# Optimization experiments

Measured on AMD Instinct MI355X. Metric: run time of the kernel, lower is better.

The kernel has to match this reference:

```python
import jax, jax.numpy as jnp
import numpy as np

EPS = 1e-5  # float32 path of the torch LayerNorm variants


def setup_inputs() -> dict:
    key = jax.random.key(0)
    ks = jax.random.split(key, 12)
    b, c, t, h, w = 2, 512, 16, 32, 32
    heads, dim_head = 8, 64
    inner = heads * dim_head            # 512
    cpb = c // 2                        # 256 (ContinuousPositionBias hidden dim)
    inner_ff = int(c * 4 * 2 / 3)       # 1365 (GEGLU FeedForward)
    s = 0.02
    return {
        "x": jax.random.normal(ks[0], (b, c, t, h, w), jnp.float32),
        "framerate": 4,
        "g_norm": jnp.ones((c,), jnp.float32),
        "Wq": jax.random.normal(ks[1], (c, inner), jnp.float32) * s,
        "Wkv": jax.random.normal(ks[2], (c, 2 * inner), jnp.float32) * s,
        "Wo": jax.random.normal(ks[3], (inner, c), jnp.float32) * s,
        "pos_emb": jax.random.normal(ks[4], (1, 30, c), jnp.float32),
        "fr_emb": jax.random.normal(ks[5], (1, 30, c), jnp.float32),
        "cpb_w1": jax.random.normal(ks[6], (1, cpb), jnp.float32) * s,
        "cpb_b1": jnp.zeros((cpb,), jnp.float32),
        "cpb_w2": jax.random.normal(ks[7], (cpb, cpb), jnp.float32) * s,
        "cpb_b2": jnp.zeros((cpb,), jnp.float32),
        "cpb_w3": jax.random.normal(ks[8], (cpb, 8), jnp.float32) * s,
        "cpb_b3": jnp.zeros((8,), jnp.float32),
        "Win": jax.random.normal(ks[9], (c, 2 * inner_ff), jnp.float32) * s,
        "chan_g": jnp.ones((inner_ff,), jnp.float32),
        "Wout": jax.random.normal(ks[10], (inner_ff, c), jnp.float32) * s,
    }


def _forward(x, framerate, g_norm, Wq, Wkv, Wo, pos_emb, fr_emb,
             cpb_w1, cpb_b1, cpb_w2, cpb_b2, cpb_w3, cpb_b3,
             Win, chan_g, Wout):
    b, c, t, hh, ww = x.shape
    heads = cpb_b3.shape[0]
    dim_head = Wq.shape[1] // heads
    scale = dim_head ** -0.5

    # ---- ContinuousPositionBias over time (num_dims=1, log_dist) ----
    pos = jnp.arange(t)
    rel = (pos[:, None] - pos[None, :])[..., None].astype(x.dtype)   # [t, t, 1]
    rel = jnp.sign(rel) * jnp.log(jnp.abs(rel) + 1.0)
    hb = jax.nn.silu(rel @ cpb_w1 + cpb_b1)
    hb = jax.nn.silu(hb @ cpb_w2 + cpb_b2)
    bias = jnp.transpose(hb @ cpb_w3 + cpb_b3, (2, 0, 1))            # [H, t, t]

    # ---- temporal attention: fold spatial dims into batch ----
    xt = jnp.transpose(x, (0, 3, 4, 2, 1)).reshape(b * hh * ww, t, c)  # [B, t, c]
    xe = xt + pos_emb[:, :t] + fr_emb[:, framerate - 1:framerate]
    # LayerNorm as written in the source: stats over dim=1 (the token axis)
    mean = jnp.mean(xe, axis=1, keepdims=True)
    var = jnp.var(xe, axis=1, keepdims=True)
    xn = (xe - mean) * jax.lax.rsqrt(jnp.maximum(var, EPS)) * g_norm

    q = (xn @ Wq).reshape(-1, t, heads, dim_head).transpose(0, 2, 1, 3)  # [B,H,t,d]
    k, v = jnp.split(xn @ Wkv, 2, axis=-1)
    k = k.reshape(-1, t, heads, dim_head).transpose(0, 2, 1, 3)
    v = v.reshape(-1, t, heads, dim_head).transpose(0, 2, 1, 3)

    sim = jnp.einsum('bhid,bhjd->bhij', q * scale, k) + bias[None]
    attn = jax.nn.softmax(sim, axis=-1)
    o = jnp.einsum('bhij,bhjd->bhid', attn, v)
    o = o.transpose(0, 2, 1, 3).reshape(-1, t, heads * dim_head) @ Wo
    xt = o + xt  # residual
    x = jnp.transpose(xt.reshape(b, hh, ww, t, c), (0, 4, 3, 1, 2))  # [b,c,t,h,w]

    # ---- GEGLU FeedForward (1x1x1 convs) with token shift over time ----
    y = jnp.einsum('bcthw,co->bothw', x, Win)
    y1, gate = jnp.split(y, 2, axis=1)
    y = y1 * jax.nn.gelu(gate, approximate=False)
    half = (y.shape[1] + 1) // 2  # torch.chunk: first chunk gets ceil
    ya, yb = y[:, :half], y[:, half:]
    yb = jnp.pad(yb, ((0, 0), (0, 0), (1, 0), (0, 0), (0, 0)))[:, :, :-1]
    y = jnp.concatenate([ya, yb], axis=1)
    m = jnp.mean(y, axis=1, keepdims=True)
    vv = jnp.var(y, axis=1, keepdims=True)
    y = (y - m) * jax.lax.rsqrt(jnp.maximum(vv, EPS)) * chan_g[None, :, None, None, None]
    y = jnp.einsum('bcthw,co->bothw', y, Wout)
    return y + x


def reference(x, framerate, g_norm, Wq, Wkv, Wo, pos_emb, fr_emb,
              cpb_w1, cpb_b1, cpb_w2, cpb_b2, cpb_w3, cpb_b3,
              Win, chan_g, Wout):
    return _forward(x, framerate, g_norm, Wq, Wkv, Wo, pos_emb, fr_emb,
                    cpb_w1, cpb_b1, cpb_w2, cpb_b2, cpb_w3, cpb_b3,
                    Win, chan_g, Wout)
```

## Files before the change

### kernel.cpp

```cpp
#include <hip/hip_runtime.h>

using u16 = unsigned short;
using f32x4 = __attribute__((ext_vector_type(4))) float;
using short8 = __attribute__((ext_vector_type(8))) short;

__device__ __forceinline__ float bf2f(u16 u) {
    union { unsigned int i; float f; } v; v.i = ((unsigned int)u) << 16; return v.f;
}
__device__ __forceinline__ u16 f2bf(float f) {
    union { float f; unsigned int i; } v; v.f = f;
    unsigned int u = v.i;
    u += 0x7fffu + ((u >> 16) & 1u);
    return (u16)(u >> 16);
}
__device__ __forceinline__ void gload16(const u16* g, u16* l) {
    __builtin_amdgcn_global_load_lds((const __attribute__((address_space(1))) void*)g,
                                     (__attribute__((address_space(3))) void*)l, 16, 0, 0);
}

__global__ __launch_bounds__(256) void prep_weights(
    const float* __restrict__ Wq, const float* __restrict__ Wkv,
    const float* __restrict__ Wo, const float* __restrict__ Win,
    const float* __restrict__ Wout, const float* __restrict__ cg,
    u16* __restrict__ wqkvt, u16* __restrict__ wot,
    u16* __restrict__ winp, u16* __restrict__ woutt)
{
    int i = blockIdx.x * 256 + threadIdx.x;
    if (i < 1536 * 512) {
        int n = i >> 9, c = i & 511;
        float v = (n < 512) ? Wq[c * 512 + n] : Wkv[c * 1024 + (n - 512)];
        wqkvt[i] = f2bf(v); return;
    }
    i -= 1536 * 512;
    if (i < 512 * 512) {
        int cc = i >> 9, k = i & 511;
        wot[i] = f2bf(Wo[k * 512 + cc]); return;
    }
    i -= 512 * 512;
    if (i < 2816 * 512) {
        int n = i >> 9, c = i & 511;
        int jj = ((n >> 5) << 4) + (n & 15);
        int gate = (n >> 4) & 1;
        float v = (jj < 1365) ? Win[c * 2730 + jj + gate * 1365] : 0.f;
        winp[i] = f2bf(v); return;
    }
    i -= 2816 * 512;
    if (i < 512 * 1408) {
        int cc = i / 1408, j = i % 1408;
        float v = (j < 1365) ? Wout[j * 512 + cc] * cg[j] : 0.f;
        woutt[i] = f2bf(v); return;
    }
}

__global__ __launch_bounds__(64) void ssum_kernel(
    const float* __restrict__ Wout, const float* __restrict__ cg, float* __restrict__ ssum)
{
    int c = blockIdx.x;
    int lane = threadIdx.x;
    float s = 0.f;
    for (int j = lane; j < 1365; j += 64) s += Wout[j * 512 + c] * cg[j];
    for (int off = 32; off; off >>= 1) s += __shfl_xor(s, off);
    if (lane == 0) ssum[c] = s;
}

__global__ __launch_bounds__(256) void bias_kernel(
    const float* __restrict__ w1, const float* __restrict__ b1,
    const float* __restrict__ w2, const float* __restrict__ b2,
    const float* __restrict__ w3, const float* __restrict__ b3,
    float* __restrict__ bias)
{
    __shared__ float h1[256], h2[256];
    int rc = blockIdx.x;
    int ti = rc >> 4, tj = rc & 15;
    int j = threadIdx.x;
    float r = (float)(ti - tj);
    float rl = (r > 0.f) ? logf(r + 1.f) : ((r < 0.f) ? -logf(1.f - r) : 0.f);
    float a = rl * w1[j] + b1[j];
    h1[j] = a / (1.f + __expf(-a));
    __syncthreads();
    float acc = b2[j];
    for (int k = 0; k < 256; ++k) acc += h1[k] * w2[k * 256 + j];
    h2[j] = acc / (1.f + __expf(-acc));
    __syncthreads();
    if (j < 8) {
        float ab = b3[j];
        for (int k = 0; k < 256; ++k) ab += h2[k] * w3[k * 8 + j];
        bias[j * 256 + ti * 16 + tj] = ab;
    }
}

__global__ __launch_bounds__(256) void k1_norm(
    const float* __restrict__ x, const int* __restrict__ frp,
    const float* __restrict__ g_norm, const float* __restrict__ pos_emb,
    const float* __restrict__ fr_emb,
    u16* __restrict__ xn, u16* __restrict__ xt)
{
    __shared__ u16 tile[256 * 34];
    const int bid = blockIdx.x;
    const int b = bid >> 10, rem = bid & 1023;
    const int hw0 = (rem >> 4) << 4;
    const int c0 = (rem & 15) << 5;
    const int tid = threadIdx.x;
    const int hwl = tid & 15, cl = tid >> 4;
    const int fr = frp[0] - 1;
    float v[2][16], mean2[2], ri2[2], gg2[2], fv2[2];
    for (int cp = 0; cp < 2; ++cp) {
        const int c = c0 + cl + (cp << 4);
        const float* xp = x + (size_t)(b * 512 + c) * 16384 + hw0 + hwl;
        const float fv = fr_emb[fr * 512 + c];
        float s1 = 0.f, s2 = 0.f;
#pragma unroll
        for (int t = 0; t < 16; ++t) {
            float xv = xp[t * 1024];
            v[cp][t] = xv;
            float xe = xv + pos_emb[t * 512 + c] + fv;
            s1 += xe; s2 += xe * xe;
        }
        float m = s1 * 0.0625f;
        float var = s2 * 0.0625f - m * m;
        mean2[cp] = m; ri2[cp] = rsqrtf(fmaxf(var, 1e-5f));
        gg2[cp] = g_norm[c]; fv2[cp] = fv;
    }
    for (int cp = 0; cp < 2; ++cp) {
        const int c = c0 + cl + (cp << 4);
#pragma unroll
        for (int t = 0; t < 16; ++t) {
            float xe = v[cp][t] + pos_emb[t * 512 + c] + fv2[cp];
            tile[((t << 4) + hwl) * 34 + cl + (cp << 4)] = f2bf((xe - mean2[cp]) * ri2[cp] * gg2[cp]);
        }
    }
    __syncthreads();
    for (int it = 0; it < 32; ++it) {
        int rowl = (tid >> 5) + (it << 3);
        int col = tid & 31;
        size_t p = (size_t)b * 16384 + (size_t)(rowl >> 4) * 1024 + hw0 + (rowl & 15);
        xn[p * 512 + c0 + col] = tile[rowl * 34 + col];
    }
    __syncthreads();
    for (int cp = 0; cp < 2; ++cp)
#pragma unroll
        for (int t = 0; t < 16; ++t)
            tile[((t << 4) + hwl) * 34 + cl + (cp << 4)] = f2bf(v[cp][t]);
    __syncthreads();
    for (int it = 0; it < 32; ++it) {
        int rowl = (tid >> 5) + (it << 3);
        int col = tid & 31;
        size_t p = (size_t)b * 16384 + (size_t)(rowl >> 4) * 1024 + hw0 + (rowl & 15);
        xt[p * 512 + c0 + col] = tile[rowl * 34 + col];
    }
}

template<int EPI>
__global__ __launch_bounds__(256, 2) void gemm_bt(
    const u16* __restrict__ A, const u16* __restrict__ B, int K, int Nb,
    u16* __restrict__ outb, float* __restrict__ outf,
    const u16* __restrict__ addb,
    const float* __restrict__ ssum, int ldOut)
{
    __shared__ u16 lds[2 * 128 * 64];
    __shared__ float smr[256];
    u16* lA = lds;
    u16* lB = lds + 128 * 64;
    const int tid = threadIdx.x, lane = tid & 63, w = tid >> 6;
    const int wr = w >> 1, wc = w & 1;
    const int cpx = gridDim.x >> 3;
    const int wgid = (blockIdx.x & 7) * cpx + (blockIdx.x >> 3);
    const int p0 = (wgid / Nb) * 128, n0 = (wgid % Nb) * 128;
    f32x4 acc[4][4] = {};
    float sst[4] = {}, sq[4] = {};
    for (int kt = 0; kt < K; kt += 64) {
        for (int i = 0; i < 4; ++i) {
            int rb = w * 4 + i;
            int r = rb * 8 + (lane >> 3);
            int cg = (lane & 7) ^ (r & 7);
            gload16(A + (size_t)(p0 + r) * K + (kt + cg * 8), lA + rb * 512);
            gload16(B + (size_t)(n0 + r) * K + (kt + cg * 8), lB + rb * 512);
        }
        __syncthreads();
#pragma unroll
        for (int kk = 0; kk < 2; ++kk) {
            short8 av[4], bv[4];
#pragma unroll
            for (int m = 0; m < 4; ++m) {
                int r = wr * 64 + m * 16 + (lane & 15);
                int cc = ((kk << 2) + (lane >> 4)) ^ (r & 7);
                av[m] = *(const short8*)(lA + r * 64 + cc * 8);
            }
#pragma unroll
            for (int n = 0; n < 4; ++n) {
                int r = wc * 64 + n * 16 + (lane & 15);
                int cc = ((kk << 2) + (lane >> 4)) ^ (r & 7);
                bv[n] = *(const short8*)(lB + r * 64 + cc * 8);
            }
            if constexpr (EPI == 3) {
                if (wc == 0) {
#pragma unroll
                    for (int m = 0; m < 4; ++m)
#pragma unroll
                        for (int j = 0; j < 8; ++j) {
                            float v = bf2f((u16)av[m][j]);
                            sst[m] += v; sq[m] += v * v;
                        }
                }
            }
#pragma unroll
            for (int m = 0; m < 4; ++m)
#pragma unroll
                for (int n = 0; n < 4; ++n)
                    acc[m][n] = __builtin_amdgcn_mfma_f32_16x16x32_bf16(av[m], bv[n], acc[m][n], 0, 0, 0);
        }
        __syncthreads();
    }

    if constexpr (EPI == 0 || EPI == 1) {
#pragma unroll
        for (int m = 0; m < 4; ++m)
#pragma unroll
            for (int n = 0; n < 4; ++n) {
                int row = p0 + wr * 64 + m * 16 + ((lane >> 4) << 2);
                int col = n0 + wc * 64 + n * 16 + (lane & 15);
#pragma unroll
                for (int r = 0; r < 4; ++r) {
                    float vv = acc[m][n][r];
                    if constexpr (EPI == 1) vv += bf2f(addb[(size_t)(row + r) * ldOut + col]);
                    outb[(size_t)(row + r) * ldOut + col] = f2bf(vv);
                }
            }
    } else if constexpr (EPI == 2) {
#pragma unroll
        for (int m = 0; m < 4; ++m)
#pragma unroll
            for (int np = 0; np < 2; ++np) {
                int nv = np << 1;
                int colBase = n0 + wc * 64 + nv * 16 + (lane & 15);
                int jj = ((colBase >> 5) << 4) + (colBase & 15);
                int rowb = p0 + wr * 64 + m * 16 + ((lane >> 4) << 2);
                int t = (rowb >> 10) & 15;
#pragma unroll
                for (int r = 0; r < 4; ++r) {
                    int p = rowb + r;
                    float vv = acc[m][nv][r], gv = acc[m][nv + 1][r];
                    float glu = vv * 0.5f * gv * (1.f + erff(gv * 0.70710678f));
                    if (jj >= 1365) {
                        outb[(size_t)p * 1408 + jj] = 0;
                    } else if (jj >= 683) {
                        if (t < 15) outb[(size_t)(p + 1024) * 1408 + jj] = f2bf(glu);
                        if (t == 0) outb[(size_t)p * 1408 + jj] = 0;
                    } else {
                        outb[(size_t)p * 1408 + jj] = f2bf(glu);
                    }
                }
            }
    } else {
        if (wc == 0) {
#pragma unroll
            for (int m = 0; m < 4; ++m) {
                float s = sst[m], q = sq[m];
                s += __shfl_xor(s, 16); q += __shfl_xor(q, 16);
                s += __shfl_xor(s, 32); q += __shfl_xor(q, 32);
                if ((lane >> 4) == 0) {
                    int row = wr * 64 + m * 16 + (lane & 15);
                    smr[row] = s; smr[128 + row] = q;
                }
            }
        }
        __syncthreads();
        if (tid < 128) {
            float mm = smr[tid] * (1.f / 1365.f);
            float var = smr[128 + tid] * (1.f / 1365.f) - mm * mm;
            smr[tid] = mm;
            smr[128 + tid] = rsqrtf(fmaxf(var, 1e-5f));
        }
        float* ldsT = (float*)lds;
        const int bb = p0 >> 14, tt = (p0 >> 10) & 15, hwb = p0 & 1023;
        float* outp = outf + (size_t)bb * 8388608 + (size_t)tt * 1024 + hwb;
        for (int cg4 = 0; cg4 < 4; ++cg4) {
            __syncthreads();
            if (wc == (cg4 >> 1)) {
#pragma unroll
                for (int m = 0; m < 4; ++m)
#pragma unroll
                    for (int nn = 0; nn < 2; ++nn) {
                        int n = ((cg4 & 1) << 1) + nn;
                        int cl2 = (nn << 4) + (lane & 15);
                        int col = n0 + wc * 64 + n * 16 + (lane & 15);
                        int rl = wr * 64 + m * 16 + ((lane >> 4) << 2);
                        float ssv = ssum[col];
#pragma unroll
                        for (int r = 0; r < 4; ++r) {
                            int p = p0 + rl + r;
                            float vv = smr[128 + rl + r] * (acc[m][n][r] - smr[rl + r] * ssv)
                                     + bf2f(addb[(size_t)p * 512 + col]);
                            ldsT[cl2 * 132 + rl + r] = vv;
                        }
                    }
            }
            __syncthreads();
#pragma unroll
            for (int e = 0; e < 16; ++e) {
                int li = e * 256 + tid;
                int cl2 = li >> 7, hwl = li & 127;
                outp[(size_t)(n0 + cg4 * 32 + cl2) * 16384 + hwl] = ldsT[cl2 * 132 + hwl];
            }
        }
    }
}

__global__ __launch_bounds__(256, 2) void attn_kernel(
    const u16* __restrict__ qkv, const float* __restrict__ bias, u16* __restrict__ o)
{
    __shared__ u16 qkvt[3 * 128 * 64];
    __shared__ float pl[128 * 17];
    __shared__ float bl[256];
    const int tid = threadIdx.x, lane = tid & 63, w = tid >> 6;
    const int pc = blockIdx.x, h = blockIdx.y;
    const int b = pc >> 7, hw0 = (pc & 127) << 3;
    bl[tid] = bias[h * 256 + tid];
    for (int i = 0; i < 12; ++i) {
        int idx = w * 12 + i;
        int s = idx >> 4, rb = idx & 15;
        int r = (rb << 3) + (lane >> 3);
        int cg = (lane & 7) ^ (r & 7);
        size_t grow = (size_t)b * 16384 + (size_t)(r >> 3) * 1024 + hw0 + (r & 7);
        gload16(qkv + grow * 1536 + s * 512 + h * 64 + cg * 8, qkvt + s * 8192 + rb * 512);
    }
    __syncthreads();
    {
        const int qrow = tid & 127, hh = tid >> 7;
        const int pix = qrow & 7, ti = qrow >> 3;
        float qv[64];
        const u16* qr = qkvt + qrow * 64;
#pragma unroll
        for (int cc = 0; cc < 8; ++cc) {
            short8 qq = *(const short8*)(qr + ((cc ^ (qrow & 7)) << 3));
#pragma unroll
            for (int j = 0; j < 8; ++j) qv[cc * 8 + j] = bf2f((u16)qq[j]);
        }
#pragma unroll
        for (int tj8 = 0; tj8 < 8; ++tj8) {
            int tj = (hh << 3) + tj8;
            int rk = (tj << 3) + pix;
            const u16* kr = qkvt + 8192 + rk * 64;
            float a = 0.f;
#pragma unroll
            for (int cc = 0; cc < 8; ++cc) {
                short8 kk = *(const short8*)(kr + ((cc ^ (rk & 7)) << 3));
#pragma unroll
                for (int j = 0; j < 8; ++j) a += qv[cc * 8 + j] * bf2f((u16)kk[j]);
            }
            pl[qrow * 17 + tj] = a * 0.125f + bl[(ti << 4) + tj];
        }
    }
    __syncthreads();
    if (tid < 128) {
        float sc[16];
#pragma unroll
        for (int j = 0; j < 16; ++j) sc[j] = pl[tid * 17 + j];
        float mx = sc[0];
#pragma unroll
        for (int j = 1; j < 16; ++j) mx = fmaxf(mx, sc[j]);
        float sum = 0.f;
#pragma unroll
        for (int j = 0; j < 16; ++j) { sc[j] = __expf(sc[j] - mx); sum += sc[j]; }
        float inv = 1.f / sum;
#pragma unroll
        for (int j = 0; j < 16; ++j) pl[tid * 17 + j] = sc[j] * inv;
    }
    __syncthreads();
    {
        const int pix = tid >> 5, dg = tid & 31;
        float v0[16], v1[16];
#pragma unroll
        for (int tj = 0; tj < 16; ++tj) {
            int rv = (tj << 3) + pix;
            unsigned int d = *(const unsigned int*)(qkvt + 16384 + rv * 64 +
                               (((dg >> 2) ^ (rv & 7)) << 3) + ((dg & 3) << 1));
            v0[tj] = bf2f((u16)(d & 0xffff));
            v1[tj] = bf2f((u16)(d >> 16));
        }
#pragma unroll
        for (int ti = 0; ti < 16; ++ti) {
            float a0 = 0.f, a1 = 0.f;
            const float* pr = pl + ((ti << 3) + pix) * 17;
#pragma unroll
            for (int tj = 0; tj < 16; ++tj) {
                float pv = pr[tj];
                a0 += pv * v0[tj];
                a1 += pv * v1[tj];
            }
            size_t p = (size_t)b * 16384 + (size_t)ti * 1024 + hw0 + pix;
            unsigned int pk = (unsigned int)f2bf(a0) | ((unsigned int)f2bf(a1) << 16);
            *(unsigned int*)(o + p * 512 + h * 64 + (dg << 1)) = pk;
        }
    }
}

extern "C" void kernel_launch(void* const* d_in, const int* in_sizes, int n_in,
                              void* d_out, int out_size, void* d_ws, size_t ws_size,
                              hipStream_t stream)
{
    const float* x       = (const float*)d_in[0];
    const int*   frp     = (const int*)d_in[1];
    const float* g_norm  = (const float*)d_in[2];
    const float* Wq      = (const float*)d_in[3];
    const float* Wkv     = (const float*)d_in[4];
    const float* Wo      = (const float*)d_in[5];
    const float* pos_emb = (const float*)d_in[6];
    const float* fr_emb  = (const float*)d_in[7];
    const float* w1      = (const float*)d_in[8];
    const float* b1      = (const float*)d_in[9];
    const float* w2      = (const float*)d_in[10];
    const float* b2      = (const float*)d_in[11];
    const float* w3      = (const float*)d_in[12];
    const float* b3      = (const float*)d_in[13];
    const float* Win     = (const float*)d_in[14];
    const float* chan_g  = (const float*)d_in[15];
    const float* Wout    = (const float*)d_in[16];

    char* ws = (char*)d_ws;
    u16*   wqkvt = (u16*)(ws + 0);
    u16*   wot   = (u16*)(ws + 1572864);
    u16*   winp  = (u16*)(ws + 2097152);
    u16*   woutt = (u16*)(ws + 4980736);
    float* ssum  = (float*)(ws + 6422528);
    float* biasb = (float*)(ws + 6424576);
    u16*   qkv   = (u16*)(ws + 8388608);
    u16*   xn    = (u16*)(ws + 109051904);
    u16*   xt    = (u16*)(ws + 142606336);
    u16*   x2    = (u16*)(ws + 176160768);
    u16*   o_att = xn;
    u16*   yg    = qkv;

    prep_weights<<<12544, 256, 0, stream>>>(Wq, Wkv, Wo, Win, Wout, chan_g, wqkvt, wot, winp, woutt);
    ssum_kernel<<<512, 64, 0, stream>>>(Wout, chan_g, ssum);
    bias_kernel<<<256, 256, 0, stream>>>(w1, b1, w2, b2, w3, b3, biasb);
    k1_norm<<<2048, 256, 0, stream>>>(x, frp, g_norm, pos_emb, fr_emb, xn, xt);
    gemm_bt<0><<<256 * 12, 256, 0, stream>>>(xn, wqkvt, 512, 12, qkv, nullptr, nullptr,
                                             nullptr, 1536);
    attn_kernel<<<dim3(256, 8), 256, 0, stream>>>(qkv, biasb, o_att);
    gemm_bt<1><<<256 * 4, 256, 0, stream>>>(o_att, wot, 512, 4, x2, nullptr, xt,
                                            nullptr, 512);
    gemm_bt<2><<<256 * 22, 256, 0, stream>>>(x2, winp, 512, 22, yg, nullptr, nullptr,
                                             nullptr, 1408);
    gemm_bt<3><<<256 * 4, 256, 0, stream>>>(yg, woutt, 1408, 4, nullptr, (float*)d_out, x2,
                                            ssum, 512);
}
```

Baseline: 437.6 us.

## Switch GEMMs to 32x32x16 MFMA and merge prep kernels into one launch

The bf16 GEMM now uses 32x32x16 MFMA tiles (2x2 per wave) instead of 16x16x32 (4x4), which reduces LDS fragment reads per k-step and changes the accumulator register layout. All epilogues (plain store, residual add, GEGLU gating, layernorm-folded output) are remapped to the new layout. The Win interleave used by GEGLU is regrouped to 32-column value/gate blocks to match. The three preprocessing kernels are merged into one launch to cut launch overhead.

```diff
diff --git a/kernel.cpp b/kernel.cpp
--- a/kernel.cpp
+++ b/kernel.cpp
@@ -1,7 +1,7 @@
 #include <hip/hip_runtime.h>
 
 using u16 = unsigned short;
-using f32x4 = __attribute__((ext_vector_type(4))) float;
+using f32x16 = __attribute__((ext_vector_type(16))) float;
 using short8 = __attribute__((ext_vector_type(8))) short;
 
 __device__ __forceinline__ float bf2f(u16 u) {
@@ -18,74 +18,74 @@
                                      (__attribute__((address_space(3))) void*)l, 16, 0, 0);
 }
 
-__global__ __launch_bounds__(256) void prep_weights(
+__global__ __launch_bounds__(256) void prep_all(
     const float* __restrict__ Wq, const float* __restrict__ Wkv,
     const float* __restrict__ Wo, const float* __restrict__ Win,
     const float* __restrict__ Wout, const float* __restrict__ cg,
-    u16* __restrict__ wqkvt, u16* __restrict__ wot,
-    u16* __restrict__ winp, u16* __restrict__ woutt)
-{
-    int i = blockIdx.x * 256 + threadIdx.x;
-    if (i < 1536 * 512) {
-        int n = i >> 9, c = i & 511;
-        float v = (n < 512) ? Wq[c * 512 + n] : Wkv[c * 1024 + (n - 512)];
-        wqkvt[i] = f2bf(v); return;
-    }
-    i -= 1536 * 512;
-    if (i < 512 * 512) {
-        int cc = i >> 9, k = i & 511;
-        wot[i] = f2bf(Wo[k * 512 + cc]); return;
-    }
-    i -= 512 * 512;
-    if (i < 2816 * 512) {
-        int n = i >> 9, c = i & 511;
-        int jj = ((n >> 5) << 4) + (n & 15);
-        int gate = (n >> 4) & 1;
-        float v = (jj < 1365) ? Win[c * 2730 + jj + gate * 1365] : 0.f;
-        winp[i] = f2bf(v); return;
-    }
-    i -= 2816 * 512;
-    if (i < 512 * 1408) {
-        int cc = i / 1408, j = i % 1408;
-        float v = (j < 1365) ? Wout[j * 512 + cc] * cg[j] : 0.f;
-        woutt[i] = f2bf(v); return;
-    }
-}
-
-__global__ __launch_bounds__(64) void ssum_kernel(
-    const float* __restrict__ Wout, const float* __restrict__ cg, float* __restrict__ ssum)
-{
-    int c = blockIdx.x;
-    int lane = threadIdx.x;
-    float s = 0.f;
-    for (int j = lane; j < 1365; j += 64) s += Wout[j * 512 + c] * cg[j];
-    for (int off = 32; off; off >>= 1) s += __shfl_xor(s, off);
-    if (lane == 0) ssum[c] = s;
-}
-
-__global__ __launch_bounds__(256) void bias_kernel(
     const float* __restrict__ w1, const float* __restrict__ b1,
     const float* __restrict__ w2, const float* __restrict__ b2,
     const float* __restrict__ w3, const float* __restrict__ b3,
-    float* __restrict__ bias)
+    u16* __restrict__ wqkvt, u16* __restrict__ wot,
+    u16* __restrict__ winp, u16* __restrict__ woutt,
+    float* __restrict__ ssum, float* __restrict__ bias)
 {
-    __shared__ float h1[256], h2[256];
-    int rc = blockIdx.x;
-    int ti = rc >> 4, tj = rc & 15;
-    int j = threadIdx.x;
-    float r = (float)(ti - tj);
-    float rl = (r > 0.f) ? logf(r + 1.f) : ((r < 0.f) ? -logf(1.f - r) : 0.f);
-    float a = rl * w1[j] + b1[j];
-    h1[j] = a / (1.f + __expf(-a));
-    __syncthreads();
-    float acc = b2[j];
-    for (int k = 0; k < 256; ++k) acc += h1[k] * w2[k * 256 + j];
-    h2[j] = acc / (1.f + __expf(-acc));
-    __syncthreads();
-    if (j < 8) {
-        float ab = b3[j];
-        for (int k = 0; k < 256; ++k) ab += h2[k] * w3[k * 8 + j];
-        bias[j * 256 + ti * 16 + tj] = ab;
+    if (blockIdx.x < 12544) {
+        int i = blockIdx.x * 256 + threadIdx.x;
+        if (i < 1536 * 512) {
+            int n = i >> 9, c = i & 511;
+            float v = (n < 512) ? Wq[c * 512 + n] : Wkv[c * 1024 + (n - 512)];
+            wqkvt[i] = f2bf(v); return;
+        }
+        i -= 1536 * 512;
+        if (i < 512 * 512) {
+            int cc = i >> 9, k = i & 511;
+            wot[i] = f2bf(Wo[k * 512 + cc]); return;
+        }
+        i -= 512 * 512;
+        if (i < 2816 * 512) {
+            int n = i >> 9, c = i & 511;
+            int g = n >> 6, within = n & 63;
+            int gate = within >> 5;
+            int jj = (g << 5) + (within & 31);
+            float v = (jj < 1365) ? Win[c * 2730 + jj + gate * 1365] : 0.f;
+            winp[i] = f2bf(v); return;
+        }
+        i -= 2816 * 512;
+        if (i < 512 * 1408) {
+            int cc = i / 1408, j = i % 1408;
+            float v = (j < 1365) ? Wout[j * 512 + cc] * cg[j] : 0.f;
+            woutt[i] = f2bf(v); return;
+        }
+        return;
+    }
+    if (blockIdx.x < 12544 + 128) {
+        int c = ((blockIdx.x - 12544) << 2) + (threadIdx.x >> 6);
+        int lane = threadIdx.x & 63;
+        float s = 0.f;
+        for (int j = lane; j < 1365; j += 64) s += Wout[j * 512 + c] * cg[j];
+        for (int off = 32; off; off >>= 1) s += __shfl_xor(s, off);
+        if (lane == 0) ssum[c] = s;
+        return;
+    }
+    {
+        __shared__ float h1[256], h2[256];
+        int rc = blockIdx.x - 12544 - 128;
+        int ti = rc >> 4, tj = rc & 15;
+        int j = threadIdx.x;
+        float r = (float)(ti - tj);
+        float rl = (r > 0.f) ? logf(r + 1.f) : ((r < 0.f) ? -logf(1.f - r) : 0.f);
+        float a = rl * w1[j] + b1[j];
+        h1[j] = a / (1.f + __expf(-a));
+        __syncthreads();
+        float acc = b2[j];
+        for (int k = 0; k < 256; ++k) acc += h1[k] * w2[k * 256 + j];
+        h2[j] = acc / (1.f + __expf(-acc));
+        __syncthreads();
+        if (j < 8) {
+            float ab = b3[j];
+            for (int k = 0; k < 256; ++k) ab += h2[k] * w3[k * 8 + j];
+            bias[j * 256 + ti * 16 + tj] = ab;
+        }
     }
 }
 
@@ -163,11 +163,24 @@
     u16* lB = lds + 128 * 64;
     const int tid = threadIdx.x, lane = tid & 63, w = tid >> 6;
     const int wr = w >> 1, wc = w & 1;
+    const int l31 = lane & 31, hi = lane >> 5;
     const int cpx = gridDim.x >> 3;
     const int wgid = (blockIdx.x & 7) * cpx + (blockIdx.x >> 3);
     const int p0 = (wgid / Nb) * 128, n0 = (wgid % Nb) * 128;
-    f32x4 acc[4][4] = {};
-    float sst[4] = {}, sq[4] = {};
+    f32x16 acc[2][2] = {};
+    float sst[2] = {}, sq[2] = {};
+
+    auto rdA = [&](int mf, int ks) -> short8 {
+        int r = wr * 64 + mf * 32 + l31;
+        int cc = ((ks << 1) + hi) ^ (r & 7);
+        return *(const short8*)(lA + r * 64 + cc * 8);
+    };
+    auto rdB = [&](int nf, int ks) -> short8 {
+        int r = wc * 64 + nf * 32 + l31;
+        int cc = ((ks << 1) + hi) ^ (r & 7);
+        return *(const short8*)(lB + r * 64 + cc * 8);
+    };
+
     for (int kt = 0; kt < K; kt += 64) {
         for (int i = 0; i < 4; ++i) {
             int rb = w * 4 + i;
@@ -178,68 +191,60 @@
         }
         __syncthreads();
 #pragma unroll
-        for (int kk = 0; kk < 2; ++kk) {
-            short8 av[4], bv[4];
-#pragma unroll
-            for (int m = 0; m < 4; ++m) {
-                int r = wr * 64 + m * 16 + (lane & 15);
-                int cc = ((kk << 2) + (lane >> 4)) ^ (r & 7);
-                av[m] = *(const short8*)(lA + r * 64 + cc * 8);
-            }
-#pragma unroll
-            for (int n = 0; n < 4; ++n) {
-                int r = wc * 64 + n * 16 + (lane & 15);
-                int cc = ((kk << 2) + (lane >> 4)) ^ (r & 7);
-                bv[n] = *(const short8*)(lB + r * 64 + cc * 8);
-            }
+        for (int ks = 0; ks < 4; ++ks) {
+            short8 av[2], bv[2];
+            av[0] = rdA(0, ks); av[1] = rdA(1, ks);
+            bv[0] = rdB(0, ks); bv[1] = rdB(1, ks);
             if constexpr (EPI == 3) {
                 if (wc == 0) {
 #pragma unroll
-                    for (int m = 0; m < 4; ++m)
+                    for (int mf = 0; mf < 2; ++mf)
 #pragma unroll
                         for (int j = 0; j < 8; ++j) {
-                            float v = bf2f((u16)av[m][j]);
-                            sst[m] += v; sq[m] += v * v;
+                            float v = bf2f((u16)av[mf][j]);
+                            sst[mf] += v; sq[mf] += v * v;
                         }
                 }
             }
 #pragma unroll
-            for (int m = 0; m < 4; ++m)
-#pragma unroll
-                for (int n = 0; n < 4; ++n)
-                    acc[m][n] = __builtin_amdgcn_mfma_f32_16x16x32_bf16(av[m], bv[n], acc[m][n], 0, 0, 0);
+            for (int mf = 0; mf < 2; ++mf)
+#pragma unroll
+                for (int nf = 0; nf < 2; ++nf)
+                    acc[mf][nf] = __builtin_amdgcn_mfma_f32_32x32x16_bf16(av[mf], bv[nf], acc[mf][nf], 0, 0, 0);
         }
         __syncthreads();
     }
 
     if constexpr (EPI == 0 || EPI == 1) {
 #pragma unroll
-        for (int m = 0; m < 4; ++m)
-#pragma unroll
-            for (int n = 0; n < 4; ++n) {
-                int row = p0 + wr * 64 + m * 16 + ((lane >> 4) << 2);
-                int col = n0 + wc * 64 + n * 16 + (lane & 15);
-#pragma unroll
-                for (int r = 0; r < 4; ++r) {
-                    float vv = acc[m][n][r];
-                    if constexpr (EPI == 1) vv += bf2f(addb[(size_t)(row + r) * ldOut + col]);
-                    outb[(size_t)(row + r) * ldOut + col] = f2bf(vv);
+        for (int mf = 0; mf < 2; ++mf)
+#pragma unroll
+            for (int nf = 0; nf < 2; ++nf) {
+                int col = n0 + wc * 64 + nf * 32 + l31;
+#pragma unroll
+                for (int q = 0; q < 4; ++q) {
+                    int row = p0 + wr * 64 + mf * 32 + q * 8 + (hi << 2);
+#pragma unroll
+                    for (int r2 = 0; r2 < 4; ++r2) {
+                        float vv = acc[mf][nf][q * 4 + r2];
+                        if constexpr (EPI == 1) vv += bf2f(addb[(size_t)(row + r2) * ldOut + col]);
+                        outb[(size_t)(row + r2) * ldOut + col] = f2bf(vv);
+                    }
                 }
             }
     } else if constexpr (EPI == 2) {
-#pragma unroll
-        for (int m = 0; m < 4; ++m)
-#pragma unroll
-            for (int np = 0; np < 2; ++np) {
-                int nv = np << 1;
-                int colBase = n0 + wc * 64 + nv * 16 + (lane & 15);
-                int jj = ((colBase >> 5) << 4) + (colBase & 15);
-                int rowb = p0 + wr * 64 + m * 16 + ((lane >> 4) << 2);
-                int t = (rowb >> 10) & 15;
-#pragma unroll
-                for (int r = 0; r < 4; ++r) {
-                    int p = rowb + r;
-                    float vv = acc[m][nv][r], gv = acc[m][nv + 1][r];
+        const int colV = n0 + wc * 64 + l31;
+        const int jj = ((colV >> 6) << 5) + (colV & 31);
+        const int t = (p0 >> 10) & 15;
+#pragma unroll
+        for (int mf = 0; mf < 2; ++mf)
+#pragma unroll
+            for (int q = 0; q < 4; ++q) {
+                int rowb = p0 + wr * 64 + mf * 32 + q * 8 + (hi << 2);
+#pragma unroll
+                for (int r2 = 0; r2 < 4; ++r2) {
+                    int p = rowb + r2;
+                    float vv = acc[mf][0][q * 4 + r2], gv = acc[mf][1][q * 4 + r2];
                     float glu = vv * 0.5f * gv * (1.f + erff(gv * 0.70710678f));
                     if (jj >= 1365) {
                         outb[(size_t)p * 1408 + jj] = 0;
@@ -254,12 +259,11 @@
     } else {
         if (wc == 0) {
 #pragma unroll
-            for (int m = 0; m < 4; ++m) {
-                float s = sst[m], q = sq[m];
-                s += __shfl_xor(s, 16); q += __shfl_xor(q, 16);
+            for (int mf = 0; mf < 2; ++mf) {
+                float s = sst[mf], q = sq[mf];
                 s += __shfl_xor(s, 32); q += __shfl_xor(q, 32);
-                if ((lane >> 4) == 0) {
-                    int row = wr * 64 + m * 16 + (lane & 15);
+                if (hi == 0) {
+                    int row = wr * 64 + mf * 32 + l31;
                     smr[row] = s; smr[128 + row] = q;
                 }
             }
@@ -277,21 +281,20 @@
         for (int cg4 = 0; cg4 < 4; ++cg4) {
             __syncthreads();
             if (wc == (cg4 >> 1)) {
-#pragma unroll
-                for (int m = 0; m < 4; ++m)
-#pragma unroll
-                    for (int nn = 0; nn < 2; ++nn) {
-                        int n = ((cg4 & 1) << 1) + nn;
-                        int cl2 = (nn << 4) + (lane & 15);
-                        int col = n0 + wc * 64 + n * 16 + (lane & 15);
-                        int rl = wr * 64 + m * 16 + ((lane >> 4) << 2);
-                        float ssv = ssum[col];
-#pragma unroll
-                        for (int r = 0; r < 4; ++r) {
-                            int p = p0 + rl + r;
-                            float vv = smr[128 + rl + r] * (acc[m][n][r] - smr[rl + r] * ssv)
+                int nf = cg4 & 1;
+                int col = n0 + wc * 64 + nf * 32 + l31;
+                float ssv = ssum[col];
+#pragma unroll
+                for (int mf = 0; mf < 2; ++mf)
+#pragma unroll
+                    for (int q = 0; q < 4; ++q) {
+                        int rl = wr * 64 + mf * 32 + q * 8 + (hi << 2);
+#pragma unroll
+                        for (int r2 = 0; r2 < 4; ++r2) {
+                            int p = p0 + rl + r2;
+                            float vv = smr[128 + rl + r2] * (acc[mf][nf][q * 4 + r2] - smr[rl + r2] * ssv)
                                      + bf2f(addb[(size_t)p * 512 + col]);
-                            ldsT[cl2 * 132 + rl + r] = vv;
+                            ldsT[l31 * 132 + rl + r2] = vv;
                         }
                     }
             }
@@ -431,9 +434,9 @@
     u16*   o_att = xn;
     u16*   yg    = qkv;
 
-    prep_weights<<<12544, 256, 0, stream>>>(Wq, Wkv, Wo, Win, Wout, chan_g, wqkvt, wot, winp, woutt);
-    ssum_kernel<<<512, 64, 0, stream>>>(Wout, chan_g, ssum);
-    bias_kernel<<<256, 256, 0, stream>>>(w1, b1, w2, b2, w3, b3, biasb);
+    prep_all<<<12544 + 128 + 256, 256, 0, stream>>>(
+        Wq, Wkv, Wo, Win, Wout, chan_g, w1, b1, w2, b2, w3, b3,
+        wqkvt, wot, winp, woutt, ssum, biasb);
     k1_norm<<<2048, 256, 0, stream>>>(x, frp, g_norm, pos_emb, fr_emb, xn, xt);
     gemm_bt<0><<<256 * 12, 256, 0, stream>>>(xn, wqkvt, 512, 12, qkv, nullptr, nullptr,
                                              nullptr, 1536);
```

New measurement: 449.3 us. 2.7% more time.

## Merge weight prep kernels and double-buffer the GEGLU GEMM

Applied to the files above, without the earlier changes.

Folds the three setup kernels (weight conversion, ssum, bias MLP) into one launch, dispatching on block index. The GEGLU feed-forward GEMM moves to a dedicated kernel that double-buffers its LDS tiles, so global-to-LDS loads for the next K step overlap MFMA work on the current one. This aims to cut launch overhead and hide load latency in the largest GEMM, at the cost of twice the LDS per block, which can limit occupancy.

```diff
diff --git a/kernel.cpp b/kernel.cpp
--- a/kernel.cpp
+++ b/kernel.cpp
@@ -17,75 +17,80 @@
     __builtin_amdgcn_global_load_lds((const __attribute__((address_space(1))) void*)g,
                                      (__attribute__((address_space(3))) void*)l, 16, 0, 0);
 }
-
-__global__ __launch_bounds__(256) void prep_weights(
+#define WAITV0() asm volatile("s_waitcnt vmcnt(0)" ::: "memory")
+__device__ __forceinline__ void barrier_() {
+    asm volatile("" ::: "memory");
+    __builtin_amdgcn_s_barrier();
+    asm volatile("" ::: "memory");
+}
+
+__global__ __launch_bounds__(256) void prep_all(
     const float* __restrict__ Wq, const float* __restrict__ Wkv,
     const float* __restrict__ Wo, const float* __restrict__ Win,
     const float* __restrict__ Wout, const float* __restrict__ cg,
-    u16* __restrict__ wqkvt, u16* __restrict__ wot,
-    u16* __restrict__ winp, u16* __restrict__ woutt)
-{
-    int i = blockIdx.x * 256 + threadIdx.x;
-    if (i < 1536 * 512) {
-        int n = i >> 9, c = i & 511;
-        float v = (n < 512) ? Wq[c * 512 + n] : Wkv[c * 1024 + (n - 512)];
-        wqkvt[i] = f2bf(v); return;
-    }
-    i -= 1536 * 512;
-    if (i < 512 * 512) {
-        int cc = i >> 9, k = i & 511;
-        wot[i] = f2bf(Wo[k * 512 + cc]); return;
-    }
-    i -= 512 * 512;
-    if (i < 2816 * 512) {
-        int n = i >> 9, c = i & 511;
-        int jj = ((n >> 5) << 4) + (n & 15);
-        int gate = (n >> 4) & 1;
-        float v = (jj < 1365) ? Win[c * 2730 + jj + gate * 1365] : 0.f;
-        winp[i] = f2bf(v); return;
-    }
-    i -= 2816 * 512;
-    if (i < 512 * 1408) {
-        int cc = i / 1408, j = i % 1408;
-        float v = (j < 1365) ? Wout[j * 512 + cc] * cg[j] : 0.f;
-        woutt[i] = f2bf(v); return;
-    }
-}
-
-__global__ __launch_bounds__(64) void ssum_kernel(
-    const float* __restrict__ Wout, const float* __restrict__ cg, float* __restrict__ ssum)
-{
-    int c = blockIdx.x;
-    int lane = threadIdx.x;
-    float s = 0.f;
-    for (int j = lane; j < 1365; j += 64) s += Wout[j * 512 + c] * cg[j];
-    for (int off = 32; off; off >>= 1) s += __shfl_xor(s, off);
-    if (lane == 0) ssum[c] = s;
-}
-
-__global__ __launch_bounds__(256) void bias_kernel(
     const float* __restrict__ w1, const float* __restrict__ b1,
     const float* __restrict__ w2, const float* __restrict__ b2,
     const float* __restrict__ w3, const float* __restrict__ b3,
-    float* __restrict__ bias)
+    u16* __restrict__ wqkvt, u16* __restrict__ wot,
+    u16* __restrict__ winp, u16* __restrict__ woutt,
+    float* __restrict__ ssum, float* __restrict__ bias)
 {
-    __shared__ float h1[256], h2[256];
-    int rc = blockIdx.x;
-    int ti = rc >> 4, tj = rc & 15;
-    int j = threadIdx.x;
-    float r = (float)(ti - tj);
-    float rl = (r > 0.f) ? logf(r + 1.f) : ((r < 0.f) ? -logf(1.f - r) : 0.f);
-    float a = rl * w1[j] + b1[j];
-    h1[j] = a / (1.f + __expf(-a));
-    __syncthreads();
-    float acc = b2[j];
-    for (int k = 0; k < 256; ++k) acc += h1[k] * w2[k * 256 + j];
-    h2[j] = acc / (1.f + __expf(-acc));
-    __syncthreads();
-    if (j < 8) {
-        float ab = b3[j];
-        for (int k = 0; k < 256; ++k) ab += h2[k] * w3[k * 8 + j];
-        bias[j * 256 + ti * 16 + tj] = ab;
+    if (blockIdx.x < 12544) {
+        int i = blockIdx.x * 256 + threadIdx.x;
+        if (i < 1536 * 512) {
+            int n = i >> 9, c = i & 511;
+            float v = (n < 512) ? Wq[c * 512 + n] : Wkv[c * 1024 + (n - 512)];
+            wqkvt[i] = f2bf(v); return;
+        }
+        i -= 1536 * 512;
+        if (i < 512 * 512) {
+            int cc = i >> 9, k = i & 511;
+            wot[i] = f2bf(Wo[k * 512 + cc]); return;
+        }
+        i -= 512 * 512;
+        if (i < 2816 * 512) {
+            int n = i >> 9, c = i & 511;
+            int jj = ((n >> 5) << 4) + (n & 15);
+            int gate = (n >> 4) & 1;
+            float v = (jj < 1365) ? Win[c * 2730 + jj + gate * 1365] : 0.f;
+            winp[i] = f2bf(v); return;
+        }
+        i -= 2816 * 512;
+        if (i < 512 * 1408) {
+            int cc = i / 1408, j = i % 1408;
+            float v = (j < 1365) ? Wout[j * 512 + cc] * cg[j] : 0.f;
+            woutt[i] = f2bf(v); return;
+        }
+        return;
+    }
+    if (blockIdx.x < 12544 + 128) {
+        int c = ((blockIdx.x - 12544) << 2) + (threadIdx.x >> 6);
+        int lane = threadIdx.x & 63;
+        float s = 0.f;
+        for (int j = lane; j < 1365; j += 64) s += Wout[j * 512 + c] * cg[j];
+        for (int off = 32; off; off >>= 1) s += __shfl_xor(s, off);
+        if (lane == 0) ssum[c] = s;
+        return;
+    }
+    {
+        __shared__ float h1[256], h2[256];
+        int rc = blockIdx.x - 12544 - 128;
+        int ti = rc >> 4, tj = rc & 15;
+        int j = threadIdx.x;
+        float r = (float)(ti - tj);
+        float rl = (r > 0.f) ? logf(r + 1.f) : ((r < 0.f) ? -logf(1.f - r) : 0.f);
+        float a = rl * w1[j] + b1[j];
+        h1[j] = a / (1.f + __expf(-a));
+        __syncthreads();
+        float acc = b2[j];
+        for (int k = 0; k < 256; ++k) acc += h1[k] * w2[k * 256 + j];
+        h2[j] = acc / (1.f + __expf(-acc));
+        __syncthreads();
+        if (j < 8) {
+            float ab = b3[j];
+            for (int k = 0; k < 256; ++k) ab += h2[k] * w3[k * 8 + j];
+            bias[j * 256 + ti * 16 + tj] = ab;
+        }
     }
 }
 
@@ -226,31 +231,6 @@
                     outb[(size_t)(row + r) * ldOut + col] = f2bf(vv);
                 }
             }
-    } else if constexpr (EPI == 2) {
-#pragma unroll
-        for (int m = 0; m < 4; ++m)
-#pragma unroll
-            for (int np = 0; np < 2; ++np) {
-                int nv = np << 1;
-                int colBase = n0 + wc * 64 + nv * 16 + (lane & 15);
-                int jj = ((colBase >> 5) << 4) + (colBase & 15);
-                int rowb = p0 + wr * 64 + m * 16 + ((lane >> 4) << 2);
-                int t = (rowb >> 10) & 15;
-#pragma unroll
-                for (int r = 0; r < 4; ++r) {
-                    int p = rowb + r;
-                    float vv = acc[m][nv][r], gv = acc[m][nv + 1][r];
-                    float glu = vv * 0.5f * gv * (1.f + erff(gv * 0.70710678f));
-                    if (jj >= 1365) {
-                        outb[(size_t)p * 1408 + jj] = 0;
-                    } else if (jj >= 683) {
-                        if (t < 15) outb[(size_t)(p + 1024) * 1408 + jj] = f2bf(glu);
-                        if (t == 0) outb[(size_t)p * 1408 + jj] = 0;
-                    } else {
-                        outb[(size_t)p * 1408 + jj] = f2bf(glu);
-                    }
-                }
-            }
     } else {
         if (wc == 0) {
 #pragma unroll
@@ -304,6 +284,87 @@
             }
         }
     }
+}
+
+__global__ __launch_bounds__(256, 2) void gemm_db_glu(
+    const u16* __restrict__ A, const u16* __restrict__ B, int K, int Nb,
+    u16* __restrict__ outb)
+{
+    __shared__ u16 lds[2][16384];
+    const int tid = threadIdx.x, lane = tid & 63, w = tid >> 6;
+    const int wr = w >> 1, wc = w & 1;
+    const int cpx = gridDim.x >> 3;
+    const int wgid = (blockIdx.x & 7) * cpx + (blockIdx.x >> 3);
+    const int p0 = (wgid / Nb) * 128, n0 = (wgid % Nb) * 128;
+
+    auto stage = [&](int buf, int kt) {
+        u16* lA = lds[buf];
+        u16* lB = lds[buf] + 8192;
+        for (int i = 0; i < 4; ++i) {
+            int rb = w * 4 + i;
+            int r = rb * 8 + (lane >> 3);
+            int cg = (lane & 7) ^ (r & 7);
+            gload16(A + (size_t)(p0 + r) * K + (kt + cg * 8), lA + rb * 512);
+            gload16(B + (size_t)(n0 + r) * K + (kt + cg * 8), lB + rb * 512);
+        }
+    };
+
+    f32x4 acc[4][4] = {};
+    stage(0, 0);
+    const int NT = K >> 6;
+    for (int i = 0; i < NT; ++i) {
+        WAITV0();
+        barrier_();
+        if (i + 1 < NT) stage((i + 1) & 1, (i + 1) << 6);
+        const u16* lA = lds[i & 1];
+        const u16* lB = lds[i & 1] + 8192;
+#pragma unroll
+        for (int kk = 0; kk < 2; ++kk) {
+            short8 av[4], bv[4];
+#pragma unroll
+            for (int m = 0; m < 4; ++m) {
+                int r = wr * 64 + m * 16 + (lane & 15);
+                int cc = ((kk << 2) + (lane >> 4)) ^ (r & 7);
+                av[m] = *(const short8*)(lA + r * 64 + cc * 8);
+            }
+#pragma unroll
+            for (int n = 0; n < 4; ++n) {
+                int r = wc * 64 + n * 16 + (lane & 15);
+                int cc = ((kk << 2) + (lane >> 4)) ^ (r & 7);
+                bv[n] = *(const short8*)(lB + r * 64 + cc * 8);
+            }
+#pragma unroll
+            for (int m = 0; m < 4; ++m)
+#pragma unroll
+                for (int n = 0; n < 4; ++n)
+                    acc[m][n] = __builtin_amdgcn_mfma_f32_16x16x32_bf16(av[m], bv[n], acc[m][n], 0, 0, 0);
+        }
+    }
+
+#pragma unroll
+    for (int m = 0; m < 4; ++m)
+#pragma unroll
+        for (int np = 0; np < 2; ++np) {
+            int nv = np << 1;
+            int colBase = n0 + wc * 64 + nv * 16 + (lane & 15);
+            int jj = ((colBase >> 5) << 4) + (colBase & 15);
+            int rowb = p0 + wr * 64 + m * 16 + ((lane >> 4) << 2);
+            int t = (rowb >> 10) & 15;
+#pragma unroll
+            for (int r = 0; r < 4; ++r) {
+                int p = rowb + r;
+                float vv = acc[m][nv][r], gv = acc[m][nv + 1][r];
+                float glu = vv * 0.5f * gv * (1.f + erff(gv * 0.70710678f));
+                if (jj >= 1365) {
+                    outb[(size_t)p * 1408 + jj] = 0;
+                } else if (jj >= 683) {
+                    if (t < 15) outb[(size_t)(p + 1024) * 1408 + jj] = f2bf(glu);
+                    if (t == 0) outb[(size_t)p * 1408 + jj] = 0;
+                } else {
+                    outb[(size_t)p * 1408 + jj] = f2bf(glu);
+                }
+            }
+        }
 }
 
 __global__ __launch_bounds__(256, 2) void attn_kernel(
@@ -431,17 +492,16 @@
     u16*   o_att = xn;
     u16*   yg    = qkv;
 
-    prep_weights<<<12544, 256, 0, stream>>>(Wq, Wkv, Wo, Win, Wout, chan_g, wqkvt, wot, winp, woutt);
-    ssum_kernel<<<512, 64, 0, stream>>>(Wout, chan_g, ssum);
-    bias_kernel<<<256, 256, 0, stream>>>(w1, b1, w2, b2, w3, b3, biasb);
+    prep_all<<<12544 + 128 + 256, 256, 0, stream>>>(
+        Wq, Wkv, Wo, Win, Wout, chan_g, w1, b1, w2, b2, w3, b3,
+        wqkvt, wot, winp, woutt, ssum, biasb);
     k1_norm<<<2048, 256, 0, stream>>>(x, frp, g_norm, pos_emb, fr_emb, xn, xt);
     gemm_bt<0><<<256 * 12, 256, 0, stream>>>(xn, wqkvt, 512, 12, qkv, nullptr, nullptr,
                                              nullptr, 1536);
     attn_kernel<<<dim3(256, 8), 256, 0, stream>>>(qkv, biasb, o_att);
     gemm_bt<1><<<256 * 4, 256, 0, stream>>>(o_att, wot, 512, 4, x2, nullptr, xt,
                                             nullptr, 512);
-    gemm_bt<2><<<256 * 22, 256, 0, stream>>>(x2, winp, 512, 22, yg, nullptr, nullptr,
-                                             nullptr, 1408);
+    gemm_db_glu<<<256 * 22, 256, 0, stream>>>(x2, winp, 512, 22, yg);
     gemm_bt<3><<<256 * 4, 256, 0, stream>>>(yg, woutt, 1408, 4, nullptr, (float*)d_out, x2,
                                             ssum, 512);
 }
```

Result: slower. 463.7 us (+6.0%).
